# Kernel tuning notes

Hardware: AMD Instinct MI355X
Metric: run time of the kernel (lower is better)

The kernel has to match this reference:

```python
import jax, jax.numpy as jnp
import numpy as np

B, S, D, EXP = 2, 2048, 128, 16
N = D * EXP  # state_dim = 2048


def setup_inputs() -> dict:
    key = jax.random.key(0)
    ks = jax.random.split(key, 11)
    s_in = 1.0 / np.sqrt(D)   # torch Linear default init bound for dim->N layers
    s_out = 1.0 / np.sqrt(N)  # for out_proj (N->dim)
    x = jax.random.normal(ks[0], (B, S, D), dtype=jnp.float32)
    W_B = jax.random.uniform(ks[1], (N, D), jnp.float32, -s_in, s_in)
    b_B = jax.random.uniform(ks[2], (N,), jnp.float32, -s_in, s_in)
    W_C = jax.random.uniform(ks[3], (N, D), jnp.float32, -s_in, s_in)
    b_C = jax.random.uniform(ks[4], (N,), jnp.float32, -s_in, s_in)
    W_dt = jax.random.uniform(ks[5], (N, D), jnp.float32, -s_in, s_in)
    b_dt = jax.random.uniform(ks[6], (N,), jnp.float32, -s_in, s_in)
    A_log = jnp.log(jax.random.uniform(ks[7], (N,), jnp.float32) * 0.5 + 0.5)
    W_out = jax.random.uniform(ks[8], (D, N), jnp.float32, -s_out, s_out)
    b_out = jax.random.uniform(ks[9], (D,), jnp.float32, -s_out, s_out)
    return {"x": x, "W_B": W_B, "b_B": b_B, "W_C": W_C, "b_C": b_C,
            "W_dt": W_dt, "b_dt": b_dt, "A_log": A_log,
            "W_out": W_out, "b_out": b_out}


def reference(x, W_B, b_B, W_C, b_C, W_dt, b_dt, A_log, W_out, b_out):
    # Featurizer projections: [B,S,D] -> [B,S,N]
    B_feat = jnp.einsum('bsd,nd->bsn', x, W_B) + b_B
    C_feat = jnp.einsum('bsd,nd->bsn', x, W_C) + b_C
    dt = jax.nn.softplus(jnp.einsum('bsd,nd->bsn', x, W_dt) + b_dt)
    A = -jnp.exp(A_log)                # [N]
    A_bar = jnp.exp(dt * A)            # [B,S,N]
    B_bar = dt * B_feat                # [B,S,N]

    # Sequential diagonal scan: h_t = A_t * h_{t-1} + B_t ; y_t = C_t * h_t
    def step(h, abc):
        a_t, b_t, c_t = abc            # each [B,N]
        h = a_t * h + b_t
        return h, c_t * h

    h0 = jnp.zeros((x.shape[0], N), dtype=x.dtype)
    xs = (jnp.swapaxes(A_bar, 0, 1),   # [S,B,N]
          jnp.swapaxes(B_bar, 0, 1),
          jnp.swapaxes(C_feat, 0, 1))
    _, ys = jax.lax.scan(step, h0, xs)  # ys: [S,B,N]
    y = jnp.swapaxes(ys, 0, 1)          # [B,S,N]
    return jnp.einsum('bsn,dn->bsd', y, W_out) + b_out
```

## Files before the change

kernel.cpp:

```cpp
#include <hip/hip_runtime.h>


#define BB 2
#define SS 2048
#define DDIM 128
#define NDIM 2048
#define TT (BB*SS)
#define NTILE (TT/16)

typedef short short8 __attribute__((ext_vector_type(8)));
typedef float floatx4 __attribute__((ext_vector_type(4)));

__device__ __forceinline__ unsigned short f2b(float f){
  unsigned u = __float_as_uint(f);
  u += 0x7FFFu + ((u >> 16) & 1u);
  return (unsigned short)(u >> 16);
}
__device__ __forceinline__ unsigned cvt_pk_bf16(float lo, float hi){
  unsigned r;
  asm("v_cvt_pk_bf16_f32 %0, %1, %2" : "=v"(r) : "v"(lo), "v"(hi));
  return r;
}
__device__ __forceinline__ float softplus_f(float v){
  return v > 15.f ? v : __logf(1.f + __expf(v));
}
__device__ __forceinline__ void pack8(const float* __restrict__ s,
                                      unsigned short* __restrict__ d){
  floatx4 v0 = *(const floatx4*)s;
  floatx4 v1 = *(const floatx4*)(s + 4);
  short8 r;
  r[0]=(short)f2b(v0[0]); r[1]=(short)f2b(v0[1]); r[2]=(short)f2b(v0[2]); r[3]=(short)f2b(v0[3]);
  r[4]=(short)f2b(v1[0]); r[5]=(short)f2b(v1[1]); r[6]=(short)f2b(v1[2]); r[7]=(short)f2b(v1[3]);
  *(short8*)d = r;
}

__global__ void prep_kernel(const float* __restrict__ x,
                            const float* __restrict__ W_B,
                            const float* __restrict__ W_C,
                            const float* __restrict__ W_dt,
                            const float* __restrict__ A_log,
                            const float* __restrict__ W_out,
                            unsigned short* __restrict__ xp,
                            unsigned short* __restrict__ Wp3,
                            unsigned short* __restrict__ Wop,
                            float* __restrict__ Aval,
                            unsigned long long* __restrict__ Sbuf){
  const int gid = blockIdx.x * blockDim.x + threadIdx.x;
  if (gid < 32768) Sbuf[gid] = 0ull;
  if (gid < 2048) Aval[gid] = -__expf(A_log[gid]);
  if (gid < 65536){
    int g = gid, tile = g >> 8, kk = (g >> 6) & 3, lane = g & 63;
    int q = lane >> 4, m = lane & 15;
    pack8(x + (size_t)(tile*16 + m)*DDIM + kk*32 + q*8, xp + (size_t)g*8);
  }
  if (gid < 98304){
    int mat = gid >> 15, g = gid & 32767;
    const float* W = (mat == 0) ? W_B : (mat == 1 ? W_dt : W_C);
    int tile = g >> 8, kk = (g >> 6) & 3, lane = g & 63;
    int q = lane >> 4, m = lane & 15;
    pack8(W + (size_t)(tile*16 + m)*DDIM + kk*32 + q*8,
          Wp3 + (size_t)mat*262144 + (size_t)g*8);
  }
  if (gid < 32768){
    int g = gid, tile = g >> 12, kk = (g >> 6) & 63, lane = g & 63;
    int q = lane >> 4, m = lane & 15;
    pack8(W_out + (size_t)(tile*16 + m)*NDIM + kk*32 + q*8, Wop + (size_t)g*8);
  }
}

__global__ __launch_bounds__(256, 2) void projscan_kernel(
    const unsigned short* __restrict__ xp,
    const unsigned short* __restrict__ Wp3,
    const float* __restrict__ b_B,
    const float* __restrict__ b_dt,
    const float* __restrict__ b_C,
    const float* __restrict__ Aval,
    unsigned long long* __restrict__ Sbuf,
    unsigned short* __restrict__ ybp){
  __shared__ unsigned short sW[3*4096];
  __shared__ float sPw[4][32], sHw[4][32];
  __shared__ float sIw[4][32];
  const int tid  = threadIdx.x;
  const int lane = tid & 63;
  const int wv   = tid >> 6;
  const int m    = lane & 15;
  const int q    = lane >> 4;
  const int p    = blockIdx.y * 16 + blockIdx.x;
  const int xcd  = p & 7;
  const int slot = p >> 3;
  const int rr   = slot & 15;
  const int j    = slot >> 4;
  const int row  = xcd*16 + rr;
  const int by   = row >> 1;
  const int bx   = (row & 1)*8 + j;
  const int n0   = by*32;
  unsigned short* sYT = sW + wv*640;

  for (int i = tid; i < 1536; i += 256){
    int mat = i >> 9, rem = i & 511;
    *(short8*)(sW + mat*4096 + rem*8) =
        *(const short8*)(Wp3 + (size_t)mat*262144 + (size_t)by*4096 + rem*8);
  }
  __syncthreads();

  float bBv[2], bDv[2], bCv[2], Avv[2];
#pragma unroll
  for (int nt = 0; nt < 2; ++nt){
    const int n = n0 + nt*16 + m;
    bBv[nt] = b_B[n]; bDv[nt] = b_dt[n]; bCv[nt] = b_C[n]; Avv[nt] = Aval[n];
  }

  unsigned ypk[4][2][2], cpk[4][2][2];
  float pe_t[4][2], he_t[4][2];
  float pa_run[2] = {1.f, 1.f}, ha_run[2] = {0.f, 0.f};

  short8 xf[2][4];
  {
    const int t0 = bx*16 + wv*4;
#pragma unroll
    for (int kk = 0; kk < 4; ++kk)
      xf[0][kk] = *(const short8*)(xp + (size_t)t0*2048 + kk*512 + lane*8);
  }

#pragma unroll
  for (int i = 0; i < 4; ++i){
    const int cur = i & 1;
    floatx4 acc[3][2];
#pragma unroll
    for (int mat = 0; mat < 3; ++mat)
#pragma unroll
      for (int nt = 0; nt < 2; ++nt)
        acc[mat][nt] = (floatx4){0.f,0.f,0.f,0.f};
#pragma unroll
    for (int nt = 0; nt < 2; ++nt)
#pragma unroll
      for (int kk = 0; kk < 4; ++kk){
        short8 wB = *(const short8*)(sW +         nt*2048 + kk*512 + lane*8);
        short8 wD = *(const short8*)(sW + 4096 +  nt*2048 + kk*512 + lane*8);
        short8 wC = *(const short8*)(sW + 8192 +  nt*2048 + kk*512 + lane*8);
        acc[0][nt] = __builtin_amdgcn_mfma_f32_16x16x32_bf16(xf[cur][kk], wB, acc[0][nt], 0, 0, 0);
        acc[1][nt] = __builtin_amdgcn_mfma_f32_16x16x32_bf16(xf[cur][kk], wD, acc[1][nt], 0, 0, 0);
        acc[2][nt] = __builtin_amdgcn_mfma_f32_16x16x32_bf16(xf[cur][kk], wC, acc[2][nt], 0, 0, 0);
      }
    if (i < 3){
      const int t1 = bx*16 + wv*4 + i + 1;
#pragma unroll
      for (int kk = 0; kk < 4; ++kk)
        xf[cur^1][kk] = *(const short8*)(xp + (size_t)t1*2048 + kk*512 + lane*8);
    }

#pragma unroll
    for (int nt = 0; nt < 2; ++nt){
      float Ar[4], Br[4], Cc[4];
#pragma unroll
      for (int r = 0; r < 4; ++r){
        float dtv = softplus_f(acc[1][nt][r] + bDv[nt]);
        Ar[r] = __expf(dtv * Avv[nt]);
        Br[r] = dtv * (acc[0][nt][r] + bBv[nt]);
        Cc[r] = acc[2][nt][r] + bCv[nt];
      }
      float P = Ar[0], H = Br[0];
#pragma unroll
      for (int r = 1; r < 4; ++r){ H = Ar[r]*H + Br[r]; P *= Ar[r]; }
      float pp = __shfl(P, (lane - 16) & 63, 64);
      float hh = __shfl(H, (lane - 16) & 63, 64);
      if (q >= 1){ H = P*hh + H; P *= pp; }
      pp = __shfl(P, (lane - 32) & 63, 64);
      hh = __shfl(H, (lane - 32) & 63, 64);
      if (q >= 2){ H = P*hh + H; P *= pp; }
      float pe = __shfl(P, (lane - 16) & 63, 64);
      float he = __shfl(H, (lane - 16) & 63, 64);
      if (q == 0){ pe = 1.f; he = 0.f; }
      float pb = __shfl(P, m + 48, 64);
      float hb = __shfl(H, m + 48, 64);

      float h = he, pa = pe;
      float ys[4], cs[4];
#pragma unroll
      for (int r = 0; r < 4; ++r){
        h = Ar[r]*h + Br[r];
        pa *= Ar[r];
        ys[r] = Cc[r]*h;
        cs[r] = Cc[r]*pa;
      }
      ypk[i][nt][0] = cvt_pk_bf16(ys[0], ys[1]);
      ypk[i][nt][1] = cvt_pk_bf16(ys[2], ys[3]);
      cpk[i][nt][0] = cvt_pk_bf16(cs[0], cs[1]);
      cpk[i][nt][1] = cvt_pk_bf16(cs[2], cs[3]);

      pe_t[i][nt] = pa_run[nt];
      he_t[i][nt] = ha_run[nt];
      ha_run[nt] = pb*ha_run[nt] + hb;
      pa_run[nt] *= pb;
    }
  }
  if (q == 0){
#pragma unroll
    for (int nt = 0; nt < 2; ++nt){
      sPw[wv][nt*16 + m] = pa_run[nt];
      sHw[wv][nt*16 + m] = ha_run[nt];
    }
  }
  __syncthreads();

  if (tid < 32){
    float Pw[4], Hw[4];
#pragma unroll
    for (int w2 = 0; w2 < 4; ++w2){ Pw[w2] = sPw[w2][tid]; Hw[w2] = sHw[w2][tid]; }
    float pb = 1.f, hb = 0.f;
#pragma unroll
    for (int w2 = 0; w2 < 4; ++w2){ hb = Pw[w2]*hb + Hw[w2]; pb *= Pw[w2]; }
    float pbc = fmaxf(pb, 1e-30f);
    __hip_atomic_store(Sbuf + (size_t)(by*16 + bx)*32 + tid,
        ((unsigned long long)__float_as_uint(pbc) << 32) |
         (unsigned long long)__float_as_uint(hb),
        __ATOMIC_RELAXED, __HIP_MEMORY_SCOPE_AGENT);
    float S = 0.f;
    const int cnt = bx & 7;
    if (cnt){
      const int j0 = bx & ~7;
      unsigned long long v0=0,v1=0,v2=0,v3=0,v4=0,v5=0,v6=0;
      unsigned got = 0;
      int spin = 0;
      const unsigned all = (1u << cnt) - 1u;
      const unsigned long long* base = Sbuf + (size_t)(by*16 + j0)*32 + tid;
      for (;;){
#define LOOKBACK(J, V)                                                          \
        if (J < cnt && !(got & (1u << J))){                                     \
          unsigned long long a = __hip_atomic_load(base + (size_t)J*32,         \
              __ATOMIC_RELAXED, __HIP_MEMORY_SCOPE_AGENT);                      \
          if ((unsigned)(a >> 32) != 0u){ V = a; got |= 1u << J; }              \
        }
        LOOKBACK(0, v0) LOOKBACK(1, v1) LOOKBACK(2, v2) LOOKBACK(3, v3)
        LOOKBACK(4, v4) LOOKBACK(5, v5) LOOKBACK(6, v6)
#undef LOOKBACK
        if (got == all) break;
        if (spin < 4)       __builtin_amdgcn_s_sleep(2);
        else if (spin < 8)  __builtin_amdgcn_s_sleep(8);
        else                __builtin_amdgcn_s_sleep(32);
        ++spin;
      }
#define COMPOSE(J, V)                                                           \
      if (J < cnt) S = __uint_as_float((unsigned)(V >> 32))*S +                 \
                       __uint_as_float((unsigned)V);
      COMPOSE(0, v0) COMPOSE(1, v1) COMPOSE(2, v2) COMPOSE(3, v3)
      COMPOSE(4, v4) COMPOSE(5, v5) COMPOSE(6, v6)
#undef COMPOSE
    }
    float s = S;
#pragma unroll
    for (int w2 = 0; w2 < 4; ++w2){
      sIw[w2][tid] = s;
      s = Pw[w2]*s + Hw[w2];
    }
  }
  __syncthreads();

  float iw[2];
#pragma unroll
  for (int nt = 0; nt < 2; ++nt) iw[nt] = sIw[wv][nt*16 + m];
#pragma unroll
  for (int i = 0; i < 4; ++i){
    const int tile = bx*16 + wv*4 + i;
#pragma unroll
    for (int nt = 0; nt < 2; ++nt){
      float it = pe_t[i][nt]*iw[nt] + he_t[i][nt];
#pragma unroll
      for (int j2 = 0; j2 < 2; ++j2){
        unsigned yp = ypk[i][nt][j2], cp = cpk[i][nt][j2];
        float y0 = __uint_as_float(yp << 16);
        float y1 = __uint_as_float(yp & 0xffff0000u);
        float c0 = __uint_as_float(cp << 16);
        float c1 = __uint_as_float(cp & 0xffff0000u);
        sYT[(q*4 + j2*2 + 0)*40 + nt*16 + m] = f2b(y0 + c0*it);
        sYT[(q*4 + j2*2 + 1)*40 + nt*16 + m] = f2b(y1 + c1*it);
      }
    }
    short8 yv = *(const short8*)&sYT[m*40 + q*8];
    *(short8*)(ybp + (size_t)tile*32768 + (size_t)by*512 + (size_t)lane*8) = yv;
  }
}

__global__ void outproj_kernel(const unsigned short* __restrict__ ybp,
                               const unsigned short* __restrict__ Wop,
                               const float* __restrict__ b_out,
                               float* __restrict__ out){
  __shared__ float red[4*2048];
  const int tid  = threadIdx.x;
  const int lane = tid & 63;
  const int wv   = tid >> 6;
  const int m    = lane & 15;
  const int q    = lane >> 4;
  const int tile = blockIdx.x;

  floatx4 acc[8];
#pragma unroll
  for (int dt = 0; dt < 8; ++dt) acc[dt] = (floatx4){0.f,0.f,0.f,0.f};

  const unsigned short* aP = ybp + (size_t)tile*32768 + lane*8;
  const unsigned short* bP = Wop + (size_t)lane*8;
#pragma unroll 4
  for (int kk = wv*16; kk < wv*16 + 16; ++kk){
    short8 af = *(const short8*)(aP + (size_t)kk*512);
#pragma unroll
    for (int dt = 0; dt < 8; ++dt){
      short8 bf = *(const short8*)(bP + (size_t)dt*32768 + (size_t)kk*512);
      acc[dt] = __builtin_amdgcn_mfma_f32_16x16x32_bf16(af, bf, acc[dt], 0, 0, 0);
    }
  }
#pragma unroll
  for (int dt = 0; dt < 8; ++dt)
#pragma unroll
    for (int r = 0; r < 4; ++r)
      red[wv*2048 + (q*4 + r)*128 + dt*16 + m] = acc[dt][r];
  __syncthreads();
#pragma unroll
  for (int i = 0; i < 8; ++i){
    int idx = i*256 + tid;
    float s = red[idx] + red[2048 + idx] + red[4096 + idx] + red[6144 + idx];
    int tl = idx >> 7, d = idx & 127;
    out[(size_t)(tile*16 + tl)*DDIM + d] = s + b_out[d];
  }
}

extern "C" void kernel_launch(void* const* d_in, const int* in_sizes, int n_in,
                              void* d_out, int out_size, void* d_ws, size_t ws_size,
                              hipStream_t stream) {
  const float* x     = (const float*)d_in[0];
  const float* W_B   = (const float*)d_in[1];
  const float* b_B   = (const float*)d_in[2];
  const float* W_C   = (const float*)d_in[3];
  const float* b_C   = (const float*)d_in[4];
  const float* W_dt  = (const float*)d_in[5];
  const float* b_dt  = (const float*)d_in[6];
  const float* A_log = (const float*)d_in[7];
  const float* W_out = (const float*)d_in[8];
  const float* b_out = (const float*)d_in[9];
  float* out = (float*)d_out;

  char* w = (char*)d_ws;
  unsigned short* xp    = (unsigned short*)(w + 0x0000000);
  unsigned short* Wp3   = (unsigned short*)(w + 0x0100000);
  unsigned short* Wop   = (unsigned short*)(w + 0x0280000);
  float*          Aval  = (float*)         (w + 0x0300000);
  unsigned short* ybp   = (unsigned short*)(w + 0x0310000);
  unsigned long long* Sbuf = (unsigned long long*)(w + 0x1310000);

  prep_kernel<<<384, 256, 0, stream>>>(
      x, W_B, W_C, W_dt, A_log, W_out, xp, Wp3, Wop, Aval, Sbuf);

  projscan_kernel<<<dim3(16, 64), 256, 0, stream>>>(
      xp, Wp3, b_B, b_dt, b_C, Aval, Sbuf, ybp);

  outproj_kernel<<<NTILE, 256, 0, stream>>>(ybp, Wop, b_out, out);
}
```

Before: 115.3 us.

## Publish per-wave scan carries and do decoupled lookback per wave without block barriers

Each wave now publishes its own 16-step chunk carry to a finer-grained global status buffer and looks back across up to 31 preceding waves itself. This removes the two __syncthreads and the single-thread block-level combine. The in-wave cross-quad scan is also rewritten from two dependent shuffle rounds into four broadcast shuffles followed by a serial composition. In exchange, each wave does longer lookback chains with more global atomic polling, and the status buffer that prep must zero grows fourfold.

```diff
diff --git a/kernel.cpp b/kernel.cpp
--- a/kernel.cpp
+++ b/kernel.cpp
@@ -46,7 +46,7 @@
                             float* __restrict__ Aval,
                             unsigned long long* __restrict__ Sbuf){
   const int gid = blockIdx.x * blockDim.x + threadIdx.x;
-  if (gid < 32768) Sbuf[gid] = 0ull;
+  if (gid < 131072) Sbuf[gid] = 0ull;
   if (gid < 2048) Aval[gid] = -__expf(A_log[gid]);
   if (gid < 65536){
     int g = gid, tile = g >> 8, kk = (g >> 6) & 3, lane = g & 63;
@@ -78,8 +78,7 @@
     unsigned long long* __restrict__ Sbuf,
     unsigned short* __restrict__ ybp){
   __shared__ unsigned short sW[3*4096];
-  __shared__ float sPw[4][32], sHw[4][32];
-  __shared__ float sIw[4][32];
+  __shared__ unsigned short sYT[4][640];
   const int tid  = threadIdx.x;
   const int lane = tid & 63;
   const int wv   = tid >> 6;
@@ -94,7 +93,8 @@
   const int by   = row >> 1;
   const int bx   = (row & 1)*8 + j;
   const int n0   = by*32;
-  unsigned short* sYT = sW + wv*640;
+  const int row32 = by*2 + (bx >> 3);
+  const int pos   = (bx & 7)*4 + wv;
 
   for (int i = tid; i < 1536; i += 256){
     int mat = i >> 9, rem = i & 511;
@@ -162,17 +162,16 @@
       float P = Ar[0], H = Br[0];
 #pragma unroll
       for (int r = 1; r < 4; ++r){ H = Ar[r]*H + Br[r]; P *= Ar[r]; }
-      float pp = __shfl(P, (lane - 16) & 63, 64);
-      float hh = __shfl(H, (lane - 16) & 63, 64);
-      if (q >= 1){ H = P*hh + H; P *= pp; }
-      pp = __shfl(P, (lane - 32) & 63, 64);
-      hh = __shfl(H, (lane - 32) & 63, 64);
-      if (q >= 2){ H = P*hh + H; P *= pp; }
-      float pe = __shfl(P, (lane - 16) & 63, 64);
-      float he = __shfl(H, (lane - 16) & 63, 64);
-      if (q == 0){ pe = 1.f; he = 0.f; }
-      float pb = __shfl(P, m + 48, 64);
-      float hb = __shfl(H, m + 48, 64);
+      float p0 = __shfl(P, m,      64), h0 = __shfl(H, m,      64);
+      float p1 = __shfl(P, m + 16, 64), h1 = __shfl(H, m + 16, 64);
+      float p2 = __shfl(P, m + 32, 64), h2 = __shfl(H, m + 32, 64);
+      float p3 = __shfl(P, m + 48, 64), h3 = __shfl(H, m + 48, 64);
+      float cp1 = p0,     ch1 = h0;
+      float cp2 = p1*cp1, ch2 = p1*ch1 + h1;
+      float cp3 = p2*cp2, ch3 = p2*ch2 + h2;
+      float pb  = p3*cp3, hb  = p3*ch3 + h3;
+      float pe = (q == 0) ? 1.f : (q == 1) ? cp1 : (q == 2) ? cp2 : cp3;
+      float he = (q == 0) ? 0.f : (q == 1) ? ch1 : (q == 2) ? ch2 : ch3;
 
       float h = he, pa = pe;
       float ys[4], cs[4];
@@ -194,71 +193,59 @@
       pa_run[nt] *= pb;
     }
   }
-  if (q == 0){
-#pragma unroll
-    for (int nt = 0; nt < 2; ++nt){
-      sPw[wv][nt*16 + m] = pa_run[nt];
-      sHw[wv][nt*16 + m] = ha_run[nt];
-    }
-  }
-  __syncthreads();
-
-  if (tid < 32){
-    float Pw[4], Hw[4];
-#pragma unroll
-    for (int w2 = 0; w2 < 4; ++w2){ Pw[w2] = sPw[w2][tid]; Hw[w2] = sHw[w2][tid]; }
-    float pb = 1.f, hb = 0.f;
-#pragma unroll
-    for (int w2 = 0; w2 < 4; ++w2){ hb = Pw[w2]*hb + Hw[w2]; pb *= Pw[w2]; }
-    float pbc = fmaxf(pb, 1e-30f);
-    __hip_atomic_store(Sbuf + (size_t)(by*16 + bx)*32 + tid,
-        ((unsigned long long)__float_as_uint(pbc) << 32) |
-         (unsigned long long)__float_as_uint(hb),
-        __ATOMIC_RELAXED, __HIP_MEMORY_SCOPE_AGENT);
-    float S = 0.f;
-    const int cnt = bx & 7;
-    if (cnt){
-      const int j0 = bx & ~7;
-      unsigned long long v0=0,v1=0,v2=0,v3=0,v4=0,v5=0,v6=0;
+
+  {
+    float a0 = __shfl(pa_run[0], lane & 15, 64);
+    float a1 = __shfl(pa_run[1], lane & 15, 64);
+    float b0 = __shfl(ha_run[0], lane & 15, 64);
+    float b1 = __shfl(ha_run[1], lane & 15, 64);
+    float pa_n = (lane & 16) ? a1 : a0;
+    float ha_n = (lane & 16) ? b1 : b0;
+    if (lane < 32){
+      float pc = fmaxf(pa_n, 1e-30f);
+      __hip_atomic_store(Sbuf + ((size_t)row32*32 + pos)*32 + lane,
+          ((unsigned long long)__float_as_uint(pc) << 32) |
+           (unsigned long long)__float_as_uint(ha_n),
+          __ATOMIC_RELAXED, __HIP_MEMORY_SCOPE_AGENT);
+    }
+  }
+
+  float S = 0.f;
+  if (lane < 32 && pos > 0){
+    const unsigned long long* base = Sbuf + (size_t)row32*1024 + lane;
+    for (int done = 0; done < pos; done += 8){
+      int cc = pos - done; if (cc > 8) cc = 8;
+      unsigned long long v0=0,v1=0,v2=0,v3=0,v4=0,v5=0,v6=0,v7=0;
       unsigned got = 0;
+      const unsigned all = (1u << cc) - 1u;
       int spin = 0;
-      const unsigned all = (1u << cnt) - 1u;
-      const unsigned long long* base = Sbuf + (size_t)(by*16 + j0)*32 + tid;
       for (;;){
 #define LOOKBACK(J, V)                                                          \
-        if (J < cnt && !(got & (1u << J))){                                     \
-          unsigned long long a = __hip_atomic_load(base + (size_t)J*32,         \
+        if (J < cc && !(got & (1u << J))){                                      \
+          unsigned long long a = __hip_atomic_load(base + (size_t)(done+J)*32,  \
               __ATOMIC_RELAXED, __HIP_MEMORY_SCOPE_AGENT);                      \
           if ((unsigned)(a >> 32) != 0u){ V = a; got |= 1u << J; }              \
         }
         LOOKBACK(0, v0) LOOKBACK(1, v1) LOOKBACK(2, v2) LOOKBACK(3, v3)
-        LOOKBACK(4, v4) LOOKBACK(5, v5) LOOKBACK(6, v6)
+        LOOKBACK(4, v4) LOOKBACK(5, v5) LOOKBACK(6, v6) LOOKBACK(7, v7)
 #undef LOOKBACK
         if (got == all) break;
-        if (spin < 4)       __builtin_amdgcn_s_sleep(2);
-        else if (spin < 8)  __builtin_amdgcn_s_sleep(8);
-        else                __builtin_amdgcn_s_sleep(32);
+        if (spin < 4) __builtin_amdgcn_s_sleep(2);
+        else          __builtin_amdgcn_s_sleep(8);
         ++spin;
       }
 #define COMPOSE(J, V)                                                           \
-      if (J < cnt) S = __uint_as_float((unsigned)(V >> 32))*S +                 \
-                       __uint_as_float((unsigned)V);
+      if (J < cc) S = __uint_as_float((unsigned)(V >> 32))*S +                  \
+                      __uint_as_float((unsigned)V);
       COMPOSE(0, v0) COMPOSE(1, v1) COMPOSE(2, v2) COMPOSE(3, v3)
-      COMPOSE(4, v4) COMPOSE(5, v5) COMPOSE(6, v6)
+      COMPOSE(4, v4) COMPOSE(5, v5) COMPOSE(6, v6) COMPOSE(7, v7)
 #undef COMPOSE
     }
-    float s = S;
-#pragma unroll
-    for (int w2 = 0; w2 < 4; ++w2){
-      sIw[w2][tid] = s;
-      s = Pw[w2]*s + Hw[w2];
-    }
-  }
-  __syncthreads();
-
+  }
   float iw[2];
 #pragma unroll
-  for (int nt = 0; nt < 2; ++nt) iw[nt] = sIw[wv][nt*16 + m];
+  for (int nt = 0; nt < 2; ++nt) iw[nt] = __shfl(S, nt*16 + m, 64);
+
 #pragma unroll
   for (int i = 0; i < 4; ++i){
     const int tile = bx*16 + wv*4 + i;
@@ -272,11 +259,11 @@
         float y1 = __uint_as_float(yp & 0xffff0000u);
         float c0 = __uint_as_float(cp << 16);
         float c1 = __uint_as_float(cp & 0xffff0000u);
-        sYT[(q*4 + j2*2 + 0)*40 + nt*16 + m] = f2b(y0 + c0*it);
-        sYT[(q*4 + j2*2 + 1)*40 + nt*16 + m] = f2b(y1 + c1*it);
-      }
-    }
-    short8 yv = *(const short8*)&sYT[m*40 + q*8];
+        sYT[wv][(q*4 + j2*2 + 0)*40 + nt*16 + m] = f2b(y0 + c0*it);
+        sYT[wv][(q*4 + j2*2 + 1)*40 + nt*16 + m] = f2b(y1 + c1*it);
+      }
+    }
+    short8 yv = *(const short8*)&sYT[wv][m*40 + q*8];
     *(short8*)(ybp + (size_t)tile*32768 + (size_t)by*512 + (size_t)lane*8) = yv;
   }
 }
@@ -346,7 +333,7 @@
   unsigned short* ybp   = (unsigned short*)(w + 0x0310000);
   unsigned long long* Sbuf = (unsigned long long*)(w + 0x1310000);
 
-  prep_kernel<<<384, 256, 0, stream>>>(
+  prep_kernel<<<512, 256, 0, stream>>>(
       x, W_B, W_C, W_dt, A_log, W_out, xp, Wp3, Wop, Aval, Sbuf);
 
   projscan_kernel<<<dim3(16, 64), 256, 0, stream>>>(
```

Measured after the change: 120.5 us. 4.5% more time.
